# Performance work log

Measured on AMD Instinct MI355X. Metric: run time of the kernel, lower is better.

## Reference

```python
import jax, jax.numpy as jnp
import numpy as np

NUM_GROUPS = 32
EPS = 1e-6


def setup_inputs() -> dict:
    key = jax.random.key(0)
    ks = jax.random.split(key, 6)
    b, c, H, W = 4, 512, 64, 64
    scale = 1.0 / np.sqrt(c)
    return {
        "x": jax.random.normal(ks[0], (b, c, H, W), dtype=jnp.float32),
        "gn_w": jnp.ones((c,), jnp.float32),
        "gn_b": jnp.zeros((c,), jnp.float32),
        "wq": jax.random.normal(ks[1], (c, c), jnp.float32) * scale,
        "bq": jnp.zeros((c,), jnp.float32),
        "wk": jax.random.normal(ks[2], (c, c), jnp.float32) * scale,
        "bk": jnp.zeros((c,), jnp.float32),
        "wv": jax.random.normal(ks[3], (c, c), jnp.float32) * scale,
        "bv": jnp.zeros((c,), jnp.float32),
        "wp": jax.random.normal(ks[4], (c, c), jnp.float32) * scale,
        "bp": jnp.zeros((c,), jnp.float32),
    }


def _group_norm(x, gamma, beta):
    b, c, H, W = x.shape
    xg = x.reshape(b, NUM_GROUPS, c // NUM_GROUPS, H, W)
    mean = xg.mean(axis=(2, 3, 4), keepdims=True)
    var = xg.var(axis=(2, 3, 4), keepdims=True)
    xn = (xg - mean) * jax.lax.rsqrt(var + EPS)
    xn = xn.reshape(b, c, H, W)
    return xn * gamma[None, :, None, None] + beta[None, :, None, None]


def reference(x, gn_w, gn_b, wq, bq, wk, bk, wv, bv, wp, bp):
    b, c, H, W = x.shape
    h = _group_norm(x, gn_w, gn_b)  # (b,c,H,W)
    hf = h.reshape(b, c, H * W)  # (b,c,n)
    # 1x1 convs == per-pixel linear maps; weight layout [out,in]
    q = jnp.einsum('oc,bcn->bno', wq, hf) + bq  # (b,n,c)
    k = jnp.einsum('oc,bcn->bon', wk, hf) + bk[None, :, None]  # (b,c,n)
    v = jnp.einsum('oc,bcn->bon', wv, hf) + bv[None, :, None]  # (b,c,n)
    attn = jnp.einsum('bnc,bcm->bnm', q, k) * (int(c) ** (-0.5))
    attn = jax.nn.softmax(attn, axis=2)  # softmax over keys m
    # A = v @ attn^T  -> (b,c,n) where A[:, :, n] = sum_m v[:,:,m] attn[n,m]
    A = jnp.einsum('bcm,bnm->bcn', v, attn)
    A = jnp.einsum('oc,bcn->bon', wp, A) + bp[None, :, None]
    return x + A.reshape(b, c, H, W)
```

## Files before the change

kernel.cpp:

```cpp
#include <hip/hip_runtime.h>

#define BATCH 4
#define CCH 512
#define NPIX 4096
#define NGRP 32
#define GSZ 16
#define GN_EPS 1e-6f

typedef __attribute__((ext_vector_type(8))) short short8;
typedef __attribute__((ext_vector_type(8))) unsigned short ushort8;
typedef __attribute__((ext_vector_type(4))) unsigned short ushort4v;
typedef __attribute__((ext_vector_type(4))) float f32x4;

__device__ inline unsigned short f2bf(float f) {
  unsigned u = __float_as_uint(f);
  unsigned r = u + 0x7fffu + ((u >> 16) & 1u);
  return (unsigned short)(r >> 16);
}
__device__ inline float bf2f(unsigned short us) {
  return __uint_as_float(((unsigned)us) << 16);
}

__global__ __launch_bounds__(256) void gn_stats(const float* __restrict__ x,
                                                float* __restrict__ stats) {
  int bg = blockIdx.x;
  const f32x4* base = (const f32x4*)(x + (size_t)bg * (GSZ * NPIX));
  float s = 0.f, ss = 0.f;
  const int n4 = GSZ * NPIX / 4;
  for (int i = threadIdx.x; i < n4; i += 256) {
    f32x4 v = base[i];
    s += v.x + v.y + v.z + v.w;
    ss += v.x * v.x + v.y * v.y + v.z * v.z + v.w * v.w;
  }
  for (int off = 32; off > 0; off >>= 1) {
    s += __shfl_xor(s, off, 64);
    ss += __shfl_xor(ss, off, 64);
  }
  __shared__ float rs[4], rss[4];
  int lane = threadIdx.x & 63, wid = threadIdx.x >> 6;
  if (lane == 0) { rs[wid] = s; rss[wid] = ss; }
  __syncthreads();
  if (threadIdx.x == 0) {
    float S = rs[0] + rs[1] + rs[2] + rs[3];
    float SS = rss[0] + rss[1] + rss[2] + rss[3];
    const float inv = 1.f / (float)(GSZ * NPIX);
    float mean = S * inv;
    float var = SS * inv - mean * mean;
    stats[bg * 2] = mean;
    stats[bg * 2 + 1] = rsqrtf(var + GN_EPS);
  }
}

__global__ __launch_bounds__(256) void gn_apply_t(const float* __restrict__ x,
                                                  const float* __restrict__ stats,
                                                  const float* __restrict__ gw,
                                                  const float* __restrict__ gb,
                                                  unsigned short* __restrict__ hT) {
  __shared__ float tile[64][65];
  int b = blockIdx.z, c0 = blockIdx.y * 64, n0 = blockIdx.x * 64;
  int t = threadIdx.x;
  int tc4 = t & 15, tr = t >> 4;
  const float* xb = x + ((size_t)b * CCH + c0) * NPIX + n0;
#pragma unroll
  for (int j = 0; j < 4; ++j) {
    int row = tr + j * 16;
    int c = c0 + row;
    float mean = stats[((size_t)b * NGRP + (c >> 4)) * 2];
    float rstd = stats[((size_t)b * NGRP + (c >> 4)) * 2 + 1];
    float ga = gw[c] * rstd;
    float be = gb[c] - mean * ga;
    f32x4 v = *(const f32x4*)(xb + (size_t)row * NPIX + tc4 * 4);
    tile[row][tc4 * 4 + 0] = v.x * ga + be;
    tile[row][tc4 * 4 + 1] = v.y * ga + be;
    tile[row][tc4 * 4 + 2] = v.z * ga + be;
    tile[row][tc4 * 4 + 3] = v.w * ga + be;
  }
  __syncthreads();
  int cc = t & 7, nr = t >> 3;
  unsigned short* outp = hT + ((size_t)b * NPIX + n0) * CCH + c0;
#pragma unroll
  for (int j = 0; j < 2; ++j) {
    int n = nr + j * 32;
    ushort8 pk;
#pragma unroll
    for (int i = 0; i < 8; ++i) pk[i] = f2bf(tile[cc * 8 + i][n]);
    *(ushort8*)(outp + (size_t)n * CCH + cc * 8) = pk;
  }
}

__global__ __launch_bounds__(256) void f32_to_bf16_4(
    const float* __restrict__ s0, const float* __restrict__ s1,
    const float* __restrict__ s2, const float* __restrict__ s3,
    unsigned short* __restrict__ dst, int n4) {
  int m = blockIdx.y;
  const float* src = (m == 0) ? s0 : (m == 1) ? s1 : (m == 2) ? s2 : s3;
  unsigned short* d = dst + (size_t)m * (CCH * CCH);
  int i = blockIdx.x * 256 + threadIdx.x;
  if (i < n4) {
    f32x4 v = ((const f32x4*)src)[i];
    ushort4v o;
    o.x = f2bf(v.x); o.y = f2bf(v.y); o.z = f2bf(v.z); o.w = f2bf(v.w);
    ((ushort4v*)d)[i] = o;
  }
}

template <int BIAS_MODE, int OUT_BF16, int RESID, int SWZ>
__global__ __launch_bounds__(256, 2) void gemm_bt(
    const unsigned short* __restrict__ A, const unsigned short* __restrict__ B,
    void* __restrict__ Cv, const float* __restrict__ bias,
    const float* __restrict__ resid, int M, int N, int K, int lda, int ldb,
    int ldc, long sA, long sB, long sC, long sR, float scale) {
  __shared__ __align__(16) unsigned short lA[128][40];
  __shared__ __align__(16) unsigned short lB[128][40];
  const int t = threadIdx.x;
  const int lane = t & 63, w = t >> 6;
  const int wr = w >> 1, wc = w & 1;
  const int fr = lane & 15, kg = lane >> 4;

  unsigned orig = blockIdx.x + gridDim.x * (blockIdx.y + gridDim.y * blockIdx.z);
  unsigned nwg = gridDim.x * gridDim.y * gridDim.z;
  unsigned tid = (orig & 7) * (nwg >> 3) + (orig >> 3);
  int mt, ntl, bz;
  if (SWZ == 2) {
    unsigned bx = tid % gridDim.x, r = tid / gridDim.x;
    ntl = (int)bx;
    mt = (int)(r % gridDim.y);
    bz = (int)(r / gridDim.y);
  } else {
    unsigned bx = tid % gridDim.x, r = tid / gridDim.x;
    mt = (int)bx;
    ntl = (int)(r % gridDim.y);
    bz = (int)(r / gridDim.y);
  }
  const int m0 = mt * 128, n0 = ntl * 128;

  const unsigned short* Abz = A + (long)bz * sA;
  const unsigned short* Bbz = B + (long)bz * sB;
  const int srow = t >> 1, skc = (t & 1) * 16;
  const unsigned short* gA = Abz + (size_t)(m0 + srow) * lda + skc;
  const unsigned short* gB = Bbz + (size_t)(n0 + srow) * ldb + skc;

  short8 a0X = *(const short8*)(gA);
  short8 a1X = *(const short8*)(gA + 8);
  short8 b0X = *(const short8*)(gB);
  short8 b1X = *(const short8*)(gB + 8);
  short8 a0Y = *(const short8*)(gA + 32);
  short8 a1Y = *(const short8*)(gA + 40);
  short8 b0Y = *(const short8*)(gB + 32);
  short8 b1Y = *(const short8*)(gB + 40);

  f32x4 acc[4][4];
  const f32x4 zero = {0.f, 0.f, 0.f, 0.f};
#pragma unroll
  for (int m = 0; m < 4; ++m)
#pragma unroll
    for (int n = 0; n < 4; ++n) acc[m][n] = zero;

  const int NT = K >> 5;
#define COMPUTE()                                                             \
  do {                                                                        \
    short8 af[4], bfr[4];                                                     \
    _Pragma("unroll") for (int m = 0; m < 4; ++m) af[m] =                     \
        *(const short8*)&lA[wr * 64 + m * 16 + fr][kg * 8];                   \
    _Pragma("unroll") for (int n = 0; n < 4; ++n) bfr[n] =                    \
        *(const short8*)&lB[wc * 64 + n * 16 + fr][kg * 8];                   \
    _Pragma("unroll") for (int m = 0; m < 4; ++m)                             \
        _Pragma("unroll") for (int n = 0; n < 4; ++n) acc[m][n] =             \
            __builtin_amdgcn_mfma_f32_16x16x32_bf16(af[m], bfr[n],            \
                                                    acc[m][n], 0, 0, 0);      \
  } while (0)

  for (int it = 0; it < NT; it += 2) {
    __syncthreads();
    *(short8*)&lA[srow][skc] = a0X;
    *(short8*)&lA[srow][skc + 8] = a1X;
    *(short8*)&lB[srow][skc] = b0X;
    *(short8*)&lB[srow][skc + 8] = b1X;
    if (it + 2 < NT) {
      a0X = *(const short8*)(gA + (it + 2) * 32);
      a1X = *(const short8*)(gA + (it + 2) * 32 + 8);
      b0X = *(const short8*)(gB + (it + 2) * 32);
      b1X = *(const short8*)(gB + (it + 2) * 32 + 8);
    }
    __syncthreads();
    COMPUTE();
    __syncthreads();
    *(short8*)&lA[srow][skc] = a0Y;
    *(short8*)&lA[srow][skc + 8] = a1Y;
    *(short8*)&lB[srow][skc] = b0Y;
    *(short8*)&lB[srow][skc + 8] = b1Y;
    if (it + 3 < NT) {
      a0Y = *(const short8*)(gA + (it + 3) * 32);
      a1Y = *(const short8*)(gA + (it + 3) * 32 + 8);
      b0Y = *(const short8*)(gB + (it + 3) * 32);
      b1Y = *(const short8*)(gB + (it + 3) * 32 + 8);
    }
    __syncthreads();
    COMPUTE();
  }
#undef COMPUTE

  const int rowbase = m0 + wr * 64 + kg * 4;
  const int colbase = n0 + wc * 64 + fr;
#pragma unroll
  for (int m = 0; m < 4; ++m) {
#pragma unroll
    for (int n = 0; n < 4; ++n) {
      int col = colbase + n * 16;
#pragma unroll
      for (int r = 0; r < 4; ++r) {
        int row = rowbase + m * 16 + r;
        float v = acc[m][n][r] * scale;
        if (BIAS_MODE == 1) v += bias[row];
        if (BIAS_MODE == 2) v += bias[col];
        if (RESID) v += resid[(size_t)bz * sR + (size_t)row * ldc + col];
        size_t idx = (size_t)bz * sC + (size_t)row * ldc + col;
        if (OUT_BF16)
          ((unsigned short*)Cv)[idx] = f2bf(v);
        else
          ((float*)Cv)[idx] = v;
      }
    }
  }
}

__global__ __launch_bounds__(512, 2) void attn_fused(
    const unsigned short* __restrict__ qg, const unsigned short* __restrict__ kgl,
    const unsigned short* __restrict__ vg, unsigned short* __restrict__ og,
    float scale) {
  __shared__ __align__(16) unsigned short Qs[64 * 512];
  __shared__ __align__(16) unsigned short Ck[2][16384];
  __shared__ __align__(16) unsigned short Ps[64 * 128];
  __shared__ float lred[2][32][4];
  __shared__ float linv[64];

  const int t = threadIdx.x;
  const int lane = t & 63;
  const int wid = t >> 6;
  const int wq = wid >> 2, wc = wid & 3;
  const int fr = lane & 15, kgp = lane >> 4;

  unsigned logical = ((unsigned)blockIdx.x & 7) * 32 + ((unsigned)blockIdx.x >> 3);
  const int bz = (int)(logical >> 6), qt = (int)(logical & 63);
  const size_t BS = (size_t)NPIX * CCH;
  const unsigned short* qb = qg + (size_t)bz * BS + (size_t)qt * 64 * CCH;
  const unsigned short* kb = kgl + (size_t)bz * BS;
  const unsigned short* vb = vg + (size_t)bz * BS;

  {
    const int row = t >> 3, c0 = (t & 7) * 64;
    const unsigned short* src = qb + (size_t)row * CCH + c0;
    const int sw = (row & 7) << 3;
#pragma unroll
    for (int i = 0; i < 8; ++i)
      *(short8*)&Qs[row * 512 + ((c0 + i * 8) ^ sw)] = *(const short8*)(src + i * 8);
  }

  const int krow = t >> 2, kseg = t & 3;
  const int kswz = (krow & 7) << 3;
  const unsigned short* gK = kb + (size_t)krow * CCH + kseg * 32;
  const unsigned short* gV = vb + (size_t)t * NPIX;

  short8 R0, R1, R2, R3;
#define LOADK(mt_, cc_)                                                       \
  do { const unsigned short* g = gK + (size_t)(mt_) * (128 * CCH) + (cc_) * 128; \
    R0 = *(const short8*)(g); R1 = *(const short8*)(g + 8);                   \
    R2 = *(const short8*)(g + 16); R3 = *(const short8*)(g + 24); } while (0)
#define LOADV(mt_, vc_)                                                       \
  do { const unsigned short* g = gV + (mt_) * 128 + (vc_) * 32;               \
    R0 = *(const short8*)(g); R1 = *(const short8*)(g + 8);                   \
    R2 = *(const short8*)(g + 16); R3 = *(const short8*)(g + 24); } while (0)
#define WRITEK(buf_)                                                          \
  do { unsigned short* d = &Ck[buf_][krow * 128];                             \
    *(short8*)(d + ((kseg * 32 + 0) ^ kswz)) = R0;                            \
    *(short8*)(d + ((kseg * 32 + 8) ^ kswz)) = R1;                            \
    *(short8*)(d + ((kseg * 32 + 16) ^ kswz)) = R2;                           \
    *(short8*)(d + ((kseg * 32 + 24) ^ kswz)) = R3; } while (0)
#define WRITEV(buf_)                                                          \
  do { unsigned short* d = &Ck[buf_][t * 8];                                  \
    *(short8*)(d + 0 * 4096) = R0; *(short8*)(d + 1 * 4096) = R1;             \
    *(short8*)(d + 2 * 4096) = R2; *(short8*)(d + 3 * 4096) = R3; } while (0)

#define PHASE_BAR()                                                           \
  do {                                                                        \
    __builtin_amdgcn_sched_barrier(0);                                        \
    asm volatile("s_waitcnt lgkmcnt(0)" ::: "memory");                        \
    __builtin_amdgcn_s_barrier();                                             \
    __builtin_amdgcn_sched_barrier(0);                                        \
  } while (0)

  f32x4 oa[2][8];
  const f32x4 zero = {0.f, 0.f, 0.f, 0.f};
#pragma unroll
  for (int i = 0; i < 2; ++i)
#pragma unroll
    for (int j = 0; j < 8; ++j) oa[i][j] = zero;
  f32x4 racc0 = zero, racc1 = zero;

  short8 ones;
#pragma unroll
  for (int i = 0; i < 8; ++i) ones[i] = (short)0x3F80;

  LOADK(0, 0);
  for (int mt = 0; mt < 32; ++mt) {
    f32x4 s00 = zero, s01 = zero, s10 = zero, s11 = zero;
#pragma unroll
    for (int ph = 0; ph < 8; ++ph) {
      const int buf = ph & 1;
      if (ph < 4) WRITEK(buf); else WRITEV(buf);
      if (ph < 3) { LOADK(mt, ph + 1); }
      else if (ph == 3) { LOADV(mt, 0); }
      else if (ph < 7) { LOADV(mt, ph - 3); }
      else { if (mt + 1 < 32) LOADK(mt + 1, 0); }
      PHASE_BAR();
      if (ph < 4) {
        __builtin_amdgcn_s_setprio(1);
#pragma unroll
        for (int kk = 0; kk < 4; ++kk) {
          const int q0 = wq * 32 + fr, q1 = wq * 32 + 16 + fr;
          const int col = ph * 128 + kk * 32 + kgp * 8;
          short8 a0 = *(const short8*)&Qs[q0 * 512 + ((col) ^ ((q0 & 7) << 3))];
          short8 a1 = *(const short8*)&Qs[q1 * 512 + ((col) ^ ((q1 & 7) << 3))];
          const int m0r = wc * 32 + fr, m1r = wc * 32 + 16 + fr;
          short8 b0 = *(const short8*)&Ck[buf][m0r * 128 +
                      ((kk * 32 + kgp * 8) ^ ((m0r & 7) << 3))];
          short8 b1 = *(const short8*)&Ck[buf][m1r * 128 +
                      ((kk * 32 + kgp * 8) ^ ((m1r & 7) << 3))];
          s00 = __builtin_amdgcn_mfma_f32_16x16x32_bf16(a0, b0, s00, 0, 0, 0);
          s01 = __builtin_amdgcn_mfma_f32_16x16x32_bf16(a0, b1, s01, 0, 0, 0);
          s10 = __builtin_amdgcn_mfma_f32_16x16x32_bf16(a1, b0, s10, 0, 0, 0);
          s11 = __builtin_amdgcn_mfma_f32_16x16x32_bf16(a1, b1, s11, 0, 0, 0);
        }
        __builtin_amdgcn_s_setprio(0);
        if (ph == 3) {
          f32x4 p00, p01, p10, p11;
#pragma unroll
          for (int r = 0; r < 4; ++r) {
            p00[r] = __expf(s00[r] * scale);
            p01[r] = __expf(s01[r] * scale);
            p10[r] = __expf(s10[r] * scale);
            p11[r] = __expf(s11[r] * scale);
          }
#pragma unroll
          for (int r = 0; r < 4; ++r) {
            const int qa = wq * 32 + kgp * 4 + r;
            const int qbr = wq * 32 + 16 + kgp * 4 + r;
            const int swa = (qa & 7) << 3, swb = (qbr & 7) << 3;
            Ps[qa * 128 + ((wc * 32 + fr) ^ swa)] = f2bf(p00[r]);
            Ps[qa * 128 + ((wc * 32 + 16 + fr) ^ swa)] = f2bf(p01[r]);
            Ps[qbr * 128 + ((wc * 32 + fr) ^ swb)] = f2bf(p10[r]);
            Ps[qbr * 128 + ((wc * 32 + 16 + fr) ^ swb)] = f2bf(p11[r]);
          }
          s00 = zero; s01 = zero; s10 = zero; s11 = zero;
        }
      } else {
        const int vc = ph - 4;
        const int q0 = wq * 32 + fr, q1 = wq * 32 + 16 + fr;
        short8 pa0 = *(const short8*)&Ps[q0 * 128 +
                     ((vc * 32 + kgp * 8) ^ ((q0 & 7) << 3))];
        short8 pa1 = *(const short8*)&Ps[q1 * 128 +
                     ((vc * 32 + kgp * 8) ^ ((q1 & 7) << 3))];
        __builtin_amdgcn_s_setprio(1);
        racc0 = __builtin_amdgcn_mfma_f32_16x16x32_bf16(pa0, ones, racc0, 0, 0, 0);
        racc1 = __builtin_amdgcn_mfma_f32_16x16x32_bf16(pa1, ones, racc1, 0, 0, 0);
#pragma unroll
        for (int fb = 0; fb < 8; ++fb) {
          const int c = wc * 128 + fb * 16 + fr;
          short8 bv = *(const short8*)&Ck[buf][kgp * 4096 + c * 8];
          oa[0][fb] = __builtin_amdgcn_mfma_f32_16x16x32_bf16(pa0, bv, oa[0][fb], 0, 0, 0);
          oa[1][fb] = __builtin_amdgcn_mfma_f32_16x16x32_bf16(pa1, bv, oa[1][fb], 0, 0, 0);
        }
        __builtin_amdgcn_s_setprio(0);
      }
    }
  }
#undef LOADK
#undef LOADV
#undef WRITEK
#undef WRITEV
#undef PHASE_BAR

  __syncthreads();
  if (fr == 0) {
#pragma unroll
    for (int r = 0; r < 4; ++r) {
      lred[wq][kgp * 4 + r][wc] = racc0[r];
      lred[wq][16 + kgp * 4 + r][wc] = racc1[r];
    }
  }
  __syncthreads();
  if (t < 64) {
    float s = lred[t >> 5][t & 31][0] + lred[t >> 5][t & 31][1] +
              lred[t >> 5][t & 31][2] + lred[t >> 5][t & 31][3];
    linv[t] = 4.f / s;
  }
  __syncthreads();
#pragma unroll
  for (int i = 0; i < 2; ++i) {
    f32x4 li = *(const f32x4*)&linv[wq * 32 + i * 16 + kgp * 4];
#pragma unroll
    for (int fb = 0; fb < 8; ++fb) {
#pragma unroll
      for (int r = 0; r < 4; ++r) {
        const int q = wq * 32 + i * 16 + kgp * 4 + r;
        const int col = wc * 128 + fb * 16 + fr;
        Qs[q * 512 + (col ^ ((q & 7) << 3))] = f2bf(oa[i][fb][r] * li[r]);
      }
    }
  }
  __syncthreads();
  {
    const int row = t >> 3, c0 = (t & 7) * 64;
    const int sw = (row & 7) << 3;
    unsigned short* dst = og + (size_t)bz * BS + ((size_t)qt * 64 + row) * CCH + c0;
#pragma unroll
    for (int i = 0; i < 8; ++i)
      *(short8*)(dst + i * 8) = *(const short8*)&Qs[row * 512 + ((c0 + i * 8) ^ sw)];
  }
}

extern "C" void kernel_launch(void* const* d_in, const int* in_sizes, int n_in,
                              void* d_out, int out_size, void* d_ws, size_t ws_size,
                              hipStream_t stream) {
  const float* x = (const float*)d_in[0];
  const float* gnw = (const float*)d_in[1];
  const float* gnb = (const float*)d_in[2];
  const float* wq = (const float*)d_in[3];
  const float* bq = (const float*)d_in[4];
  const float* wk = (const float*)d_in[5];
  const float* bk = (const float*)d_in[6];
  const float* wv = (const float*)d_in[7];
  const float* bv = (const float*)d_in[8];
  const float* wp = (const float*)d_in[9];
  const float* bp = (const float*)d_in[10];
  float* out = (float*)d_out;

  const size_t BS = (size_t)NPIX * CCH;

  char* ws = (char*)d_ws;
  float* stats = (float*)ws;
  unsigned short* hT = (unsigned short*)(ws + 1024);
  unsigned short* Abuf = hT;
  unsigned short* qb = hT + BATCH * BS;
  unsigned short* kTb = qb + BATCH * BS;
  unsigned short* vb = kTb + BATCH * BS;
  unsigned short* wqb = vb + BATCH * BS;
  unsigned short* wkb = wqb + CCH * CCH;
  unsigned short* wvb = wkb + CCH * CCH;
  unsigned short* wpb = wvb + CCH * CCH;
  size_t need = (size_t)((char*)(wpb + CCH * CCH) - ws);
  if (ws_size < need) return;

  f32_to_bf16_4<<<dim3(256, 4), 256, 0, stream>>>(wq, wk, wv, wp, wqb,
                                                  CCH * CCH / 4);

  gn_stats<<<BATCH * NGRP, 256, 0, stream>>>(x, stats);
  gn_apply_t<<<dim3(NPIX / 64, CCH / 64, BATCH), 256, 0, stream>>>(x, stats, gnw,
                                                                   gnb, hT);

  gemm_bt<2, 1, 0, 2><<<dim3(4, 32, BATCH), 256, 0, stream>>>(
      hT, wqb, qb, bq, nullptr, NPIX, CCH, CCH, CCH, CCH, CCH, (long)BS, 0,
      (long)BS, 0, 1.f);
  gemm_bt<2, 1, 0, 2><<<dim3(4, 32, BATCH), 256, 0, stream>>>(
      hT, wkb, kTb, bk, nullptr, NPIX, CCH, CCH, CCH, CCH, CCH, (long)BS, 0,
      (long)BS, 0, 1.f);
  gemm_bt<1, 1, 0, 0><<<dim3(4, 32, BATCH), 256, 0, stream>>>(
      wvb, hT, vb, bv, nullptr, CCH, NPIX, CCH, CCH, CCH, NPIX, 0, (long)BS,
      (long)BS, 0, 1.f);

  const float sscale = 0.044194173824159216f;
  attn_fused<<<BATCH * 64, 512, 0, stream>>>(qb, kTb, vb, Abuf, sscale);

  gemm_bt<1, 0, 1, 0><<<dim3(4, 32, BATCH), 256, 0, stream>>>(
      wpb, Abuf, out, bp, x, CCH, NPIX, CCH, CCH, CCH, NPIX, 0, (long)BS,
      (long)BS, (long)BS, 1.f);
}
```

Measured before the change: 316.2 us.

## Load V fragments directly from global into registers, bypassing LDS staging

V tiles are no longer staged through shared memory. Each lane now loads its MFMA B-operand fragments for P·V straight from global memory into registers, prefetching the next 32-column chunk while the current MFMAs run. This removes four LDS write phases and their barriers per key tile, leaving one barrier before the PV stage. In exchange it uses more VGPRs and issues less coalesced global loads with exposed latency, and the next K tile's load now happens after PV instead of overlapping with it.

```diff
diff --git a/kernel.cpp b/kernel.cpp
--- a/kernel.cpp
+++ b/kernel.cpp
@@ -259,15 +259,11 @@
   const int krow = t >> 2, kseg = t & 3;
   const int kswz = (krow & 7) << 3;
   const unsigned short* gK = kb + (size_t)krow * CCH + kseg * 32;
-  const unsigned short* gV = vb + (size_t)t * NPIX;
+  const unsigned short* gV0 = vb + (size_t)(wc * 128 + fr) * NPIX + kgp * 8;
 
   short8 R0, R1, R2, R3;
 #define LOADK(mt_, cc_)                                                       \
   do { const unsigned short* g = gK + (size_t)(mt_) * (128 * CCH) + (cc_) * 128; \
-    R0 = *(const short8*)(g); R1 = *(const short8*)(g + 8);                   \
-    R2 = *(const short8*)(g + 16); R3 = *(const short8*)(g + 24); } while (0)
-#define LOADV(mt_, vc_)                                                       \
-  do { const unsigned short* g = gV + (mt_) * 128 + (vc_) * 32;               \
     R0 = *(const short8*)(g); R1 = *(const short8*)(g + 8);                   \
     R2 = *(const short8*)(g + 16); R3 = *(const short8*)(g + 24); } while (0)
 #define WRITEK(buf_)                                                          \
@@ -276,10 +272,6 @@
     *(short8*)(d + ((kseg * 32 + 8) ^ kswz)) = R1;                            \
     *(short8*)(d + ((kseg * 32 + 16) ^ kswz)) = R2;                           \
     *(short8*)(d + ((kseg * 32 + 24) ^ kswz)) = R3; } while (0)
-#define WRITEV(buf_)                                                          \
-  do { unsigned short* d = &Ck[buf_][t * 8];                                  \
-    *(short8*)(d + 0 * 4096) = R0; *(short8*)(d + 1 * 4096) = R1;             \
-    *(short8*)(d + 2 * 4096) = R2; *(short8*)(d + 3 * 4096) = R3; } while (0)
 
 #define PHASE_BAR()                                                           \
   do {                                                                        \
@@ -289,6 +281,9 @@
     __builtin_amdgcn_sched_barrier(0);                                        \
   } while (0)
 
+#define VLOAD(mt_, vc_, fb_)                                                  \
+  (*(const short8*)(gV0 + (size_t)(fb_) * (16 * NPIX) + (mt_)*128 + (vc_)*32))
+
   f32x4 oa[2][8];
   const f32x4 zero = {0.f, 0.f, 0.f, 0.f};
 #pragma unroll
@@ -300,84 +295,83 @@
   short8 ones;
 #pragma unroll
   for (int i = 0; i < 8; ++i) ones[i] = (short)0x3F80;
+
+  short8 vf[8];
 
   LOADK(0, 0);
   for (int mt = 0; mt < 32; ++mt) {
     f32x4 s00 = zero, s01 = zero, s10 = zero, s11 = zero;
 #pragma unroll
-    for (int ph = 0; ph < 8; ++ph) {
+    for (int ph = 0; ph < 4; ++ph) {
       const int buf = ph & 1;
-      if (ph < 4) WRITEK(buf); else WRITEV(buf);
-      if (ph < 3) { LOADK(mt, ph + 1); }
-      else if (ph == 3) { LOADV(mt, 0); }
-      else if (ph < 7) { LOADV(mt, ph - 3); }
-      else { if (mt + 1 < 32) LOADK(mt + 1, 0); }
+      WRITEK(buf);
+      if (ph < 3) LOADK(mt, ph + 1);
       PHASE_BAR();
-      if (ph < 4) {
-        __builtin_amdgcn_s_setprio(1);
-#pragma unroll
-        for (int kk = 0; kk < 4; ++kk) {
-          const int q0 = wq * 32 + fr, q1 = wq * 32 + 16 + fr;
-          const int col = ph * 128 + kk * 32 + kgp * 8;
-          short8 a0 = *(const short8*)&Qs[q0 * 512 + ((col) ^ ((q0 & 7) << 3))];
-          short8 a1 = *(const short8*)&Qs[q1 * 512 + ((col) ^ ((q1 & 7) << 3))];
-          const int m0r = wc * 32 + fr, m1r = wc * 32 + 16 + fr;
-          short8 b0 = *(const short8*)&Ck[buf][m0r * 128 +
-                      ((kk * 32 + kgp * 8) ^ ((m0r & 7) << 3))];
-          short8 b1 = *(const short8*)&Ck[buf][m1r * 128 +
-                      ((kk * 32 + kgp * 8) ^ ((m1r & 7) << 3))];
-          s00 = __builtin_amdgcn_mfma_f32_16x16x32_bf16(a0, b0, s00, 0, 0, 0);
-          s01 = __builtin_amdgcn_mfma_f32_16x16x32_bf16(a0, b1, s01, 0, 0, 0);
-          s10 = __builtin_amdgcn_mfma_f32_16x16x32_bf16(a1, b0, s10, 0, 0, 0);
-          s11 = __builtin_amdgcn_mfma_f32_16x16x32_bf16(a1, b1, s11, 0, 0, 0);
+      __builtin_amdgcn_s_setprio(1);
+#pragma unroll
+      for (int kk = 0; kk < 4; ++kk) {
+        const int q0 = wq * 32 + fr, q1 = wq * 32 + 16 + fr;
+        const int col = ph * 128 + kk * 32 + kgp * 8;
+        short8 a0 = *(const short8*)&Qs[q0 * 512 + ((col) ^ ((q0 & 7) << 3))];
+        short8 a1 = *(const short8*)&Qs[q1 * 512 + ((col) ^ ((q1 & 7) << 3))];
+        const int m0r = wc * 32 + fr, m1r = wc * 32 + 16 + fr;
+        short8 b0 = *(const short8*)&Ck[buf][m0r * 128 +
+                    ((kk * 32 + kgp * 8) ^ ((m0r & 7) << 3))];
+        short8 b1 = *(const short8*)&Ck[buf][m1r * 128 +
+                    ((kk * 32 + kgp * 8) ^ ((m1r & 7) << 3))];
+        s00 = __builtin_amdgcn_mfma_f32_16x16x32_bf16(a0, b0, s00, 0, 0, 0);
+        s01 = __builtin_amdgcn_mfma_f32_16x16x32_bf16(a0, b1, s01, 0, 0, 0);
+        s10 = __builtin_amdgcn_mfma_f32_16x16x32_bf16(a1, b0, s10, 0, 0, 0);
+        s11 = __builtin_amdgcn_mfma_f32_16x16x32_bf16(a1, b1, s11, 0, 0, 0);
+      }
+      __builtin_amdgcn_s_setprio(0);
+      if (ph == 3) {
+#pragma unroll
+        for (int fb = 0; fb < 8; ++fb) vf[fb] = VLOAD(mt, 0, fb);
+        f32x4 p00, p01, p10, p11;
+#pragma unroll
+        for (int r = 0; r < 4; ++r) {
+          p00[r] = __expf(s00[r] * scale);
+          p01[r] = __expf(s01[r] * scale);
+          p10[r] = __expf(s10[r] * scale);
+          p11[r] = __expf(s11[r] * scale);
         }
-        __builtin_amdgcn_s_setprio(0);
-        if (ph == 3) {
-          f32x4 p00, p01, p10, p11;
-#pragma unroll
-          for (int r = 0; r < 4; ++r) {
-            p00[r] = __expf(s00[r] * scale);
-            p01[r] = __expf(s01[r] * scale);
-            p10[r] = __expf(s10[r] * scale);
-            p11[r] = __expf(s11[r] * scale);
-          }
-#pragma unroll
-          for (int r = 0; r < 4; ++r) {
-            const int qa = wq * 32 + kgp * 4 + r;
-            const int qbr = wq * 32 + 16 + kgp * 4 + r;
-            const int swa = (qa & 7) << 3, swb = (qbr & 7) << 3;
-            Ps[qa * 128 + ((wc * 32 + fr) ^ swa)] = f2bf(p00[r]);
-            Ps[qa * 128 + ((wc * 32 + 16 + fr) ^ swa)] = f2bf(p01[r]);
-            Ps[qbr * 128 + ((wc * 32 + fr) ^ swb)] = f2bf(p10[r]);
-            Ps[qbr * 128 + ((wc * 32 + 16 + fr) ^ swb)] = f2bf(p11[r]);
-          }
-          s00 = zero; s01 = zero; s10 = zero; s11 = zero;
+#pragma unroll
+        for (int r = 0; r < 4; ++r) {
+          const int qa = wq * 32 + kgp * 4 + r;
+          const int qbr = wq * 32 + 16 + kgp * 4 + r;
+          const int swa = (qa & 7) << 3, swb = (qbr & 7) << 3;
+          Ps[qa * 128 + ((wc * 32 + fr) ^ swa)] = f2bf(p00[r]);
+          Ps[qa * 128 + ((wc * 32 + 16 + fr) ^ swa)] = f2bf(p01[r]);
+          Ps[qbr * 128 + ((wc * 32 + fr) ^ swb)] = f2bf(p10[r]);
+          Ps[qbr * 128 + ((wc * 32 + 16 + fr) ^ swb)] = f2bf(p11[r]);
         }
-      } else {
-        const int vc = ph - 4;
-        const int q0 = wq * 32 + fr, q1 = wq * 32 + 16 + fr;
-        short8 pa0 = *(const short8*)&Ps[q0 * 128 +
-                     ((vc * 32 + kgp * 8) ^ ((q0 & 7) << 3))];
-        short8 pa1 = *(const short8*)&Ps[q1 * 128 +
-                     ((vc * 32 + kgp * 8) ^ ((q1 & 7) << 3))];
-        __builtin_amdgcn_s_setprio(1);
-        racc0 = __builtin_amdgcn_mfma_f32_16x16x32_bf16(pa0, ones, racc0, 0, 0, 0);
-        racc1 = __builtin_amdgcn_mfma_f32_16x16x32_bf16(pa1, ones, racc1, 0, 0, 0);
-#pragma unroll
-        for (int fb = 0; fb < 8; ++fb) {
-          const int c = wc * 128 + fb * 16 + fr;
-          short8 bv = *(const short8*)&Ck[buf][kgp * 4096 + c * 8];
-          oa[0][fb] = __builtin_amdgcn_mfma_f32_16x16x32_bf16(pa0, bv, oa[0][fb], 0, 0, 0);
-          oa[1][fb] = __builtin_amdgcn_mfma_f32_16x16x32_bf16(pa1, bv, oa[1][fb], 0, 0, 0);
-        }
-        __builtin_amdgcn_s_setprio(0);
       }
     }
+    PHASE_BAR();
+#pragma unroll
+    for (int vc = 0; vc < 4; ++vc) {
+      const int q0 = wq * 32 + fr, q1 = wq * 32 + 16 + fr;
+      short8 pa0 = *(const short8*)&Ps[q0 * 128 +
+                   ((vc * 32 + kgp * 8) ^ ((q0 & 7) << 3))];
+      short8 pa1 = *(const short8*)&Ps[q1 * 128 +
+                   ((vc * 32 + kgp * 8) ^ ((q1 & 7) << 3))];
+      __builtin_amdgcn_s_setprio(1);
+      racc0 = __builtin_amdgcn_mfma_f32_16x16x32_bf16(pa0, ones, racc0, 0, 0, 0);
+      racc1 = __builtin_amdgcn_mfma_f32_16x16x32_bf16(pa1, ones, racc1, 0, 0, 0);
+#pragma unroll
+      for (int fb = 0; fb < 8; ++fb) {
+        oa[0][fb] = __builtin_amdgcn_mfma_f32_16x16x32_bf16(pa0, vf[fb], oa[0][fb], 0, 0, 0);
+        oa[1][fb] = __builtin_amdgcn_mfma_f32_16x16x32_bf16(pa1, vf[fb], oa[1][fb], 0, 0, 0);
+        if (vc < 3) vf[fb] = VLOAD(mt, vc + 1, fb);
+      }
+      __builtin_amdgcn_s_setprio(0);
+    }
+    if (mt + 1 < 32) LOADK(mt + 1, 0);
   }
 #undef LOADK
-#undef LOADV
 #undef WRITEK
-#undef WRITEV
+#undef VLOAD
 #undef PHASE_BAR
 
   __syncthreads();
```

After: 450.0 us. +42.3%, slower.
